# Kernel tuning notes

Hardware: AMD Instinct MI355X
Metric: run time of the kernel (lower is better)

## Reference

```python
import jax, jax.numpy as jnp
import numpy as np

NQ = 4   # qubits (2x2 patch)
NL = 3   # circuit layers
B = 262144


def _apply_ry(state, theta, q):
    # state: (B, 2,2,2,2) complex64; theta: scalar or (B,1,1,1) float32
    st = jnp.moveaxis(state, q + 1, -1)
    c = jnp.cos(theta * 0.5).astype(jnp.float32)
    s = jnp.sin(theta * 0.5).astype(jnp.float32)
    s0, s1 = st[..., 0], st[..., 1]
    new = jnp.stack([c * s0 - s * s1, s * s0 + c * s1], axis=-1)
    return jnp.moveaxis(new, -1, q + 1)


def _apply_rz(state, theta, q):
    # RZ = diag(exp(-i theta/2), exp(+i theta/2))
    st = jnp.moveaxis(state, q + 1, -1)
    p1 = jnp.exp(0.5j * theta.astype(jnp.complex64)).astype(jnp.complex64)
    new = jnp.stack([st[..., 0] * jnp.conj(p1), st[..., 1] * p1], axis=-1)
    return jnp.moveaxis(new, -1, q + 1)


def _apply_cnot(state, c, t):
    # control c, target t: flip target amplitudes where control == 1
    st = jnp.moveaxis(state, (c + 1, t + 1), (-2, -1))
    new = jnp.stack([st[..., 0, :], st[..., 1, ::-1]], axis=-2)
    return jnp.moveaxis(new, (-2, -1), (c + 1, t + 1))


def _circuit(x, params):
    b = x.shape[0]
    # |0000> initial state
    state = jnp.zeros((b,) + (2,) * NQ, jnp.complex64)
    state = state.at[(slice(None),) + (0,) * NQ].set(1.0)
    # data encoding: RY(x_i) on wire i (batched angles)
    for i in range(NQ):
        state = _apply_ry(state, x[:, i].reshape(-1, 1, 1, 1), i)
    # variational layers
    for l in range(NL):
        for i in range(NQ):
            state = _apply_ry(state, params[l, i, 0], i)
            state = _apply_rz(state, params[l, i, 1], i)
        for i in range(NQ - 1):
            state = _apply_cnot(state, i, i + 1)
    # <Z_i> = P(qubit i = 0) - P(qubit i = 1)
    probs = state.real ** 2 + state.imag ** 2  # (B,2,2,2,2) float32
    zs = []
    for i in range(NQ):
        other = tuple(a for a in range(1, NQ + 1) if a != i + 1)
        p = probs.sum(axis=other)  # (B, 2)
        zs.append(p[:, 0] - p[:, 1])
    return jnp.stack(zs, axis=-1)  # (B, 4)


def setup_inputs() -> dict:
    key = jax.random.key(0)
    kx, kp = jax.random.split(key)
    x = jax.random.normal(kx, (B, NQ), dtype=jnp.float32)
    params = jax.random.normal(kp, (NL, NQ, 3), dtype=jnp.float32)
    return {"x": x, "params": params}


def reference(x, params):
    return _circuit(x, params)
```

## Files before the change

### kernel.cpp

```cpp
#include <hip/hip_runtime.h>

template<int Q>
__device__ __forceinline__ void apply_ry(float (&sr)[16], float (&si)[16], float c, float s) {
    constexpr int m = 1 << (3 - Q);
    #pragma unroll
    for (int idx = 0; idx < 16; ++idx) {
        if (!(idx & m)) {
            const int j = idx | m;
            float ar = sr[idx], ai = si[idx], br = sr[j], bi = si[j];
            sr[idx] = c * ar - s * br;  si[idx] = c * ai - s * bi;
            sr[j]   = s * ar + c * br;  si[j]   = s * ai + c * bi;
        }
    }
}
template<int Q>
__device__ __forceinline__ void apply_rz(float (&sr)[16], float (&si)[16], float c, float s) {
    constexpr int m = 1 << (3 - Q);
    #pragma unroll
    for (int idx = 0; idx < 16; ++idx) {
        float r = sr[idx], i_ = si[idx];
        if (idx & m) { sr[idx] = c * r - s * i_;  si[idx] = c * i_ + s * r; }
        else         { sr[idx] = c * r + s * i_;  si[idx] = c * i_ - s * r; }
    }
}
template<int C, int T>
__device__ __forceinline__ void apply_cnot(float (&sr)[16], float (&si)[16]) {
    constexpr int mc = 1 << (3 - C), mt = 1 << (3 - T);
    #pragma unroll
    for (int idx = 0; idx < 16; ++idx) {
        if ((idx & mc) && !(idx & mt)) {
            const int j = idx | mt;
            float tr = sr[idx], ti = si[idx];
            sr[idx] = sr[j];  si[idx] = si[j];
            sr[j] = tr;       si[j] = ti;
        }
    }
}

__global__ void trig_kernel(const float* __restrict__ params, float* __restrict__ trig) {
    int j = threadIdx.x;
    if (j >= 12) return;
    float th_ry = params[j * 3 + 0];
    float th_rz = params[j * 3 + 1];
    float cy, sy, cz, sz;
    sincosf(0.5f * th_ry, &sy, &cy);
    sincosf(0.5f * th_rz, &sz, &cz);
    trig[j * 4 + 0] = cy;  trig[j * 4 + 1] = sy;
    trig[j * 4 + 2] = cz;  trig[j * 4 + 3] = sz;
}

template<bool USE_TRIG>
__global__ __launch_bounds__(256) void qsim_kernel(const float* __restrict__ x,
                                                   const float* __restrict__ trig,
                                                   const float* __restrict__ params,
                                                   float* __restrict__ out, int n) {
    int b = blockIdx.x * blockDim.x + threadIdx.x;
    if (b >= n) return;

    float4 xr = reinterpret_cast<const float4*>(x)[b];
    float c0, s0, c1, s1, c2, s2, c3, s3;
    __sincosf(0.5f * xr.x, &s0, &c0);
    __sincosf(0.5f * xr.y, &s1, &c1);
    __sincosf(0.5f * xr.z, &s2, &c2);
    __sincosf(0.5f * xr.w, &s3, &c3);

    float p01[4] = {c0 * c1, c0 * s1, s0 * c1, s0 * s1};
    float p23[4] = {c2 * c3, c2 * s3, s2 * c3, s2 * s3};
    float sr[16], si[16];
    #pragma unroll
    for (int i = 0; i < 16; ++i) { sr[i] = p01[i >> 2] * p23[i & 3]; si[i] = 0.0f; }

    #pragma unroll
    for (int l = 0; l < 3; ++l) {
        float t[16];
        if (USE_TRIG) {
            #pragma unroll
            for (int k = 0; k < 16; ++k) t[k] = trig[l * 16 + k];
        } else {
            #pragma unroll
            for (int i = 0; i < 4; ++i) {
                float th_ry = params[(l * 4 + i) * 3 + 0];
                float th_rz = params[(l * 4 + i) * 3 + 1];
                __sincosf(0.5f * th_ry, &t[i * 4 + 1], &t[i * 4 + 0]);
                __sincosf(0.5f * th_rz, &t[i * 4 + 3], &t[i * 4 + 2]);
            }
        }
        apply_ry<0>(sr, si, t[0],  t[1]);   apply_rz<0>(sr, si, t[2],  t[3]);
        apply_ry<1>(sr, si, t[4],  t[5]);   apply_rz<1>(sr, si, t[6],  t[7]);
        apply_ry<2>(sr, si, t[8],  t[9]);   apply_rz<2>(sr, si, t[10], t[11]);
        apply_ry<3>(sr, si, t[12], t[13]);  apply_rz<3>(sr, si, t[14], t[15]);
        apply_cnot<0, 1>(sr, si);
        apply_cnot<1, 2>(sr, si);
        apply_cnot<2, 3>(sr, si);
    }

    float z0 = 0.f, z1 = 0.f, z2 = 0.f, z3 = 0.f;
    #pragma unroll
    for (int i = 0; i < 16; ++i) {
        float p = sr[i] * sr[i] + si[i] * si[i];
        z0 += (i & 8) ? -p : p;
        z1 += (i & 4) ? -p : p;
        z2 += (i & 2) ? -p : p;
        z3 += (i & 1) ? -p : p;
    }

    float4 o;
    o.x = z0;  o.y = z1;  o.z = z2;  o.w = z3;
    reinterpret_cast<float4*>(out)[b] = o;
}

extern "C" void kernel_launch(void* const* d_in, const int* in_sizes, int n_in,
                              void* d_out, int out_size, void* d_ws, size_t ws_size,
                              hipStream_t stream) {
    const float* x      = (const float*)d_in[0];
    const float* params = (const float*)d_in[1];
    float* out          = (float*)d_out;
    int n = in_sizes[0] / 4;
    int blocks = (n + 255) / 256;

    if (ws_size >= 48 * sizeof(float)) {
        float* trig = (float*)d_ws;
        hipLaunchKernelGGL(trig_kernel, dim3(1), dim3(64), 0, stream, params, trig);
        hipLaunchKernelGGL((qsim_kernel<true>), dim3(blocks), dim3(256), 0, stream,
                           x, trig, params, out, n);
    } else {
        hipLaunchKernelGGL((qsim_kernel<false>), dim3(blocks), dim3(256), 0, stream,
                           x, (const float*)nullptr, params, out, n);
    }
}
```

Measured before the change: 71.14 us.

## Simplify circuit algebraically and drop separate trig kernel launch

Applies circuit identities to shorten the per-sample work. The first-layer RY is merged into the encoding RY by adding the angles, and the state stays a product state until the first CNOT, so it is built directly from per-qubit complex vectors. The last layer's RZ gates are dropped because diagonal phases followed by CNOT permutations do not change Z expectations. The trig precompute kernel is removed, and each thread computes the parameter sin/cos itself, which avoids an extra launch at the cost of redundant per-thread trig.

```diff
diff --git a/kernel.cpp b/kernel.cpp
--- a/kernel.cpp
+++ b/kernel.cpp
@@ -37,75 +37,89 @@
     }
 }
 
-__global__ void trig_kernel(const float* __restrict__ params, float* __restrict__ trig) {
-    int j = threadIdx.x;
-    if (j >= 12) return;
-    float th_ry = params[j * 3 + 0];
-    float th_rz = params[j * 3 + 1];
-    float cy, sy, cz, sz;
-    sincosf(0.5f * th_ry, &sy, &cy);
-    sincosf(0.5f * th_rz, &sz, &cz);
-    trig[j * 4 + 0] = cy;  trig[j * 4 + 1] = sy;
-    trig[j * 4 + 2] = cz;  trig[j * 4 + 3] = sz;
-}
-
-template<bool USE_TRIG>
 __global__ __launch_bounds__(256) void qsim_kernel(const float* __restrict__ x,
-                                                   const float* __restrict__ trig,
                                                    const float* __restrict__ params,
                                                    float* __restrict__ out, int n) {
     int b = blockIdx.x * blockDim.x + threadIdx.x;
     if (b >= n) return;
 
+    float cf[4], sf[4];
+    float c1y[4], s1y[4];
+    float c1z[4], s1z[4];
+    float c2y[4], s2y[4];
+    #pragma unroll
+    for (int i = 0; i < 4; ++i) {
+        __sincosf(params[0 * 12 + i * 3 + 1],        &sf[i],  &cf[i]);
+        __sincosf(0.5f * params[1 * 12 + i * 3 + 0], &s1y[i], &c1y[i]);
+        __sincosf(0.5f * params[1 * 12 + i * 3 + 1], &s1z[i], &c1z[i]);
+        __sincosf(0.5f * params[2 * 12 + i * 3 + 0], &s2y[i], &c2y[i]);
+    }
+
     float4 xr = reinterpret_cast<const float4*>(x)[b];
-    float c0, s0, c1, s1, c2, s2, c3, s3;
-    __sincosf(0.5f * xr.x, &s0, &c0);
-    __sincosf(0.5f * xr.y, &s1, &c1);
-    __sincosf(0.5f * xr.z, &s2, &c2);
-    __sincosf(0.5f * xr.w, &s3, &c3);
+    float cy[4], sy[4];
+    __sincosf(0.5f * (xr.x + params[0 * 12 + 0 * 3 + 0]), &sy[0], &cy[0]);
+    __sincosf(0.5f * (xr.y + params[0 * 12 + 1 * 3 + 0]), &sy[1], &cy[1]);
+    __sincosf(0.5f * (xr.z + params[0 * 12 + 2 * 3 + 0]), &sy[2], &cy[2]);
+    __sincosf(0.5f * (xr.w + params[0 * 12 + 3 * 3 + 0]), &sy[3], &cy[3]);
+    float v1r[4], v1i[4];
+    #pragma unroll
+    for (int i = 0; i < 4; ++i) { v1r[i] = sy[i] * cf[i]; v1i[i] = sy[i] * sf[i]; }
 
-    float p01[4] = {c0 * c1, c0 * s1, s0 * c1, s0 * s1};
-    float p23[4] = {c2 * c3, c2 * s3, s2 * c3, s2 * s3};
+    float pr[4], pi_[4], qr[4], qi[4];
+    pr[0] = cy[0] * cy[1];                          pi_[0] = 0.0f;
+    pr[1] = cy[0] * v1r[1];                         pi_[1] = cy[0] * v1i[1];
+    pr[2] = v1r[0] * cy[1];                         pi_[2] = v1i[0] * cy[1];
+    pr[3] = v1r[0] * v1r[1] - v1i[0] * v1i[1];      pi_[3] = v1r[0] * v1i[1] + v1i[0] * v1r[1];
+    qr[0] = cy[2] * cy[3];                          qi[0] = 0.0f;
+    qr[1] = cy[2] * v1r[3];                         qi[1] = cy[2] * v1i[3];
+    qr[2] = v1r[2] * cy[3];                         qi[2] = v1i[2] * cy[3];
+    qr[3] = v1r[2] * v1r[3] - v1i[2] * v1i[3];      qi[3] = v1r[2] * v1i[3] + v1i[2] * v1r[3];
+
     float sr[16], si[16];
     #pragma unroll
-    for (int i = 0; i < 16; ++i) { sr[i] = p01[i >> 2] * p23[i & 3]; si[i] = 0.0f; }
+    for (int p = 0; p < 4; ++p)
+        #pragma unroll
+        for (int q = 0; q < 4; ++q) {
+            sr[p * 4 + q] = pr[p] * qr[q] - pi_[p] * qi[q];
+            si[p * 4 + q] = pr[p] * qi[q] + pi_[p] * qr[q];
+        }
 
+    apply_cnot<0, 1>(sr, si);
+    apply_cnot<1, 2>(sr, si);
+    apply_cnot<2, 3>(sr, si);
+
+    apply_ry<0>(sr, si, c1y[0], s1y[0]);  apply_rz<0>(sr, si, c1z[0], s1z[0]);
+    apply_ry<1>(sr, si, c1y[1], s1y[1]);  apply_rz<1>(sr, si, c1z[1], s1z[1]);
+    apply_ry<2>(sr, si, c1y[2], s1y[2]);  apply_rz<2>(sr, si, c1z[2], s1z[2]);
+    apply_ry<3>(sr, si, c1y[3], s1y[3]);  apply_rz<3>(sr, si, c1z[3], s1z[3]);
+    apply_cnot<0, 1>(sr, si);
+    apply_cnot<1, 2>(sr, si);
+    apply_cnot<2, 3>(sr, si);
+
+    apply_ry<0>(sr, si, c2y[0], s2y[0]);
+    apply_ry<1>(sr, si, c2y[1], s2y[1]);
+    apply_ry<2>(sr, si, c2y[2], s2y[2]);
+    apply_ry<3>(sr, si, c2y[3], s2y[3]);
+    apply_cnot<0, 1>(sr, si);
+    apply_cnot<1, 2>(sr, si);
+    apply_cnot<2, 3>(sr, si);
+
+    float p16[16];
     #pragma unroll
-    for (int l = 0; l < 3; ++l) {
-        float t[16];
-        if (USE_TRIG) {
-            #pragma unroll
-            for (int k = 0; k < 16; ++k) t[k] = trig[l * 16 + k];
-        } else {
-            #pragma unroll
-            for (int i = 0; i < 4; ++i) {
-                float th_ry = params[(l * 4 + i) * 3 + 0];
-                float th_rz = params[(l * 4 + i) * 3 + 1];
-                __sincosf(0.5f * th_ry, &t[i * 4 + 1], &t[i * 4 + 0]);
-                __sincosf(0.5f * th_rz, &t[i * 4 + 3], &t[i * 4 + 2]);
-            }
-        }
-        apply_ry<0>(sr, si, t[0],  t[1]);   apply_rz<0>(sr, si, t[2],  t[3]);
-        apply_ry<1>(sr, si, t[4],  t[5]);   apply_rz<1>(sr, si, t[6],  t[7]);
-        apply_ry<2>(sr, si, t[8],  t[9]);   apply_rz<2>(sr, si, t[10], t[11]);
-        apply_ry<3>(sr, si, t[12], t[13]);  apply_rz<3>(sr, si, t[14], t[15]);
-        apply_cnot<0, 1>(sr, si);
-        apply_cnot<1, 2>(sr, si);
-        apply_cnot<2, 3>(sr, si);
-    }
+    for (int i = 0; i < 16; ++i) p16[i] = sr[i] * sr[i] + si[i] * si[i];
+    float s8[8], d8[8];
+    #pragma unroll
+    for (int i = 0; i < 8; ++i) { s8[i] = p16[2 * i] + p16[2 * i + 1];
+                                  d8[i] = p16[2 * i] - p16[2 * i + 1]; }
+    float z3 = (d8[0] + d8[1]) + (d8[2] + d8[3]) + ((d8[4] + d8[5]) + (d8[6] + d8[7]));
+    float z2 = (s8[0] - s8[1]) + (s8[2] - s8[3]) + ((s8[4] - s8[5]) + (s8[6] - s8[7]));
+    float t4[4];
+    #pragma unroll
+    for (int i = 0; i < 4; ++i) t4[i] = s8[2 * i] + s8[2 * i + 1];
+    float z1 = (t4[0] - t4[1]) + (t4[2] - t4[3]);
+    float z0 = (t4[0] + t4[1]) - (t4[2] + t4[3]);
 
-    float z0 = 0.f, z1 = 0.f, z2 = 0.f, z3 = 0.f;
-    #pragma unroll
-    for (int i = 0; i < 16; ++i) {
-        float p = sr[i] * sr[i] + si[i] * si[i];
-        z0 += (i & 8) ? -p : p;
-        z1 += (i & 4) ? -p : p;
-        z2 += (i & 2) ? -p : p;
-        z3 += (i & 1) ? -p : p;
-    }
-
-    float4 o;
-    o.x = z0;  o.y = z1;  o.z = z2;  o.w = z3;
+    float4 o;  o.x = z0;  o.y = z1;  o.z = z2;  o.w = z3;
     reinterpret_cast<float4*>(out)[b] = o;
 }
 
@@ -117,14 +131,5 @@
     float* out          = (float*)d_out;
     int n = in_sizes[0] / 4;
     int blocks = (n + 255) / 256;
-
-    if (ws_size >= 48 * sizeof(float)) {
-        float* trig = (float*)d_ws;
-        hipLaunchKernelGGL(trig_kernel, dim3(1), dim3(64), 0, stream, params, trig);
-        hipLaunchKernelGGL((qsim_kernel<true>), dim3(blocks), dim3(256), 0, stream,
-                           x, trig, params, out, n);
-    } else {
-        hipLaunchKernelGGL((qsim_kernel<false>), dim3(blocks), dim3(256), 0, stream,
-                           x, (const float*)nullptr, params, out, n);
-    }
+    hipLaunchKernelGGL(qsim_kernel, dim3(blocks), dim3(256), 0, stream, x, params, out, n);
 }
```

Measured after the change: 62.39 us. 1.14x faster.
